# Kernel tuning notes

Measured on AMD Instinct MI355X. Metric: run time of the kernel, lower is better.

Reference implementation:

```python
import jax, jax.numpy as jnp
import numpy as np

B, T = 64, 256
IN, HID, OUT = 512, 1024, 256
NUM_DOMAINS = 20

def setup_inputs() -> dict:
    key = jax.random.key(0)
    k1, k2, k3, k4 = jax.random.split(key, 4)
    x = jax.random.normal(k1, (B, T, IN), dtype=jnp.float32)
    hetero_info = jax.random.randint(k2, (B, 2), 0, NUM_DOMAINS, dtype=jnp.int64)
    # embedding tables init N(0, 0.02) as in the torch module
    fc1_table = 0.02 * jax.random.normal(k3, (NUM_DOMAINS, IN * HID + HID), dtype=jnp.float32)
    fc2_table = 0.02 * jax.random.normal(k4, (NUM_DOMAINS, HID * OUT + OUT), dtype=jnp.float32)
    return {"x": x, "hetero_info": hetero_info, "fc1_table": fc1_table, "fc2_table": fc2_table}

def reference(x, hetero_info, fc1_table, fc2_table):
    domain_id = hetero_info[:, 0].astype(jnp.int32)
    Bn = domain_id.shape[0]
    fc1_param = fc1_table[domain_id]                     # (B, IN*HID + HID)
    w1 = fc1_param[:, : IN * HID].reshape(Bn, IN, HID)   # (B, IN, HID)
    b1 = fc1_param[:, IN * HID:].reshape(Bn, 1, HID)
    fc2_param = fc2_table[domain_id]                     # (B, HID*OUT + OUT)
    w2 = fc2_param[:, : HID * OUT].reshape(Bn, HID, OUT) # (B, HID, OUT)
    b2 = fc2_param[:, HID * OUT:].reshape(Bn, 1, OUT)
    h = jnp.einsum('bti,bih->bth', x, w1) + b1
    h = jax.nn.gelu(h, approximate=False)  # torch nn.GELU default = exact erf
    out = jnp.einsum('bth,bho->bto', h, w2) + b2
    return out
```

## Files before the change

kernel.cpp:

```cpp
#include <hip/hip_runtime.h>
#include <math.h>

#define B_  64
#define T_  256
#define IN_ 512
#define HID_ 1024
#define OUT_ 256
#define NDOM 20

typedef __bf16 bf16_t;
typedef __bf16 bf16x8 __attribute__((ext_vector_type(8)));
typedef float  f32x4  __attribute__((ext_vector_type(4)));

#define LSTR 40

__device__ __forceinline__ unsigned f2bf_bits(float f) {
    unsigned u = __builtin_bit_cast(unsigned, f);
    return (u + 0x7FFFu + ((u >> 16) & 1u)) >> 16;
}
__device__ __forceinline__ unsigned pack_bf16x2(float x, float y) {
    return f2bf_bits(x) | (f2bf_bits(y) << 16);
}

template<int K, int N>
__global__ __launch_bounds__(256) void cvt_transpose(
    const float* __restrict__ table,
    bf16_t*      __restrict__ Wt,
    float*       __restrict__ BiasOut)
{
    const int d  = blockIdx.z;
    const float* W = table + (size_t)d * ((size_t)K * N + N);
    const int n0 = blockIdx.x * 64;
    const int k0 = blockIdx.y * 64;
    const int tid = threadIdx.x;

    __shared__ float t[64][65];

    #pragma unroll
    for (int r = 0; r < 4; ++r) {
        const int kl = (tid >> 4) + r * 16;
        const int nl = (tid & 15) * 4;
        float4 v = *(const float4*)(W + (size_t)(k0 + kl) * N + n0 + nl);
        t[kl][nl + 0] = v.x; t[kl][nl + 1] = v.y;
        t[kl][nl + 2] = v.z; t[kl][nl + 3] = v.w;
    }
    __syncthreads();

    bf16_t* Wtd = Wt + (size_t)d * K * N;
    #pragma unroll
    for (int r = 0; r < 4; ++r) {
        const int nl = (tid >> 4) + r * 16;
        const int k4 = (tid & 15) * 4;
        uint2 p;
        p.x = pack_bf16x2(t[k4 + 0][nl], t[k4 + 1][nl]);
        p.y = pack_bf16x2(t[k4 + 2][nl], t[k4 + 3][nl]);
        *(uint2*)(Wtd + (size_t)(n0 + nl) * K + k0 + k4) = p;
    }

    if (blockIdx.y == 0 && tid < 64)
        BiasOut[(size_t)d * N + n0 + tid] = W[(size_t)K * N + n0 + tid];
}

template<int N_ALL, int K, int BM, int BN, bool GELU, bool A_BF16, typename OUT_T>
__global__ __launch_bounds__(256) void mfma_bgemm(
    const void*   __restrict__ Ain,
    const bf16_t* __restrict__ Wt,
    const float*  __restrict__ Bias,
    const int*    __restrict__ hetero,
    OUT_T*        __restrict__ Out)
{
    constexpr int FI = BM / 32;
    constexpr int FJ = BN / 32;

    const int b = blockIdx.z;
    const int d = hetero[2 * b];
    const bf16_t* W    = Wt + (size_t)d * N_ALL * K;
    const float*  bias = Bias + (size_t)d * N_ALL;

    const int n0 = blockIdx.x * BN;
    const int m0 = blockIdx.y * BM;

    __shared__ bf16_t LdsA[BM * LSTR];
    __shared__ bf16_t LdsB[BN * LSTR];

    const int tid  = threadIdx.x;
    const int wave = tid >> 6;
    const int lane = tid & 63;
    const int l16  = lane & 15;
    const int quad = lane >> 4;
    const int wm   = (wave >> 1) * (BM / 2);
    const int wn   = (wave & 1) * (BN / 2);

    f32x4 acc[FI][FJ] = {};

    for (int kk = 0; kk < K; kk += 32) {
        if constexpr (A_BF16) {
            const bf16_t* A = (const bf16_t*)Ain + (size_t)b * 256 * K;
            const int kc = (tid & 3) * 8;
            #pragma unroll
            for (int r = 0; r < BM / 64; ++r) {
                const int m = (tid >> 2) + r * 64;
                *(uint4*)&LdsA[m * LSTR + kc] =
                    *(const uint4*)(A + (size_t)(m0 + m) * K + kk + kc);
            }
        } else {
            const float* A = (const float*)Ain + (size_t)b * 256 * K;
            const int kc = (tid & 7) * 4;
            #pragma unroll
            for (int r = 0; r < BM / 32; ++r) {
                const int m = (tid >> 3) + r * 32;
                float4 v = *(const float4*)(A + (size_t)(m0 + m) * K + kk + kc);
                uint2 p;
                p.x = pack_bf16x2(v.x, v.y);
                p.y = pack_bf16x2(v.z, v.w);
                *(uint2*)&LdsA[m * LSTR + kc] = p;
            }
        }
        {
            const int kc = (tid & 3) * 8;
            #pragma unroll
            for (int r = 0; r < BN / 64; ++r) {
                const int n = (tid >> 2) + r * 64;
                *(uint4*)&LdsB[n * LSTR + kc] =
                    *(const uint4*)(W + (size_t)(n0 + n) * K + kk + kc);
            }
        }
        __syncthreads();

        bf16x8 af[FI], bfg[FJ];
        #pragma unroll
        for (int i = 0; i < FI; ++i)
            af[i] = *(const bf16x8*)&LdsA[(wm + i * 16 + l16) * LSTR + quad * 8];
        #pragma unroll
        for (int j = 0; j < FJ; ++j)
            bfg[j] = *(const bf16x8*)&LdsB[(wn + j * 16 + l16) * LSTR + quad * 8];
        #pragma unroll
        for (int i = 0; i < FI; ++i)
            #pragma unroll
            for (int j = 0; j < FJ; ++j)
                acc[i][j] = __builtin_amdgcn_mfma_f32_16x16x32_bf16(af[i], bfg[j], acc[i][j], 0, 0, 0);
        __syncthreads();
    }

    #pragma unroll
    for (int j = 0; j < FJ; ++j) {
        const int n = n0 + wn + j * 16 + l16;
        const float bia = bias[n];
        #pragma unroll
        for (int i = 0; i < FI; ++i) {
            const int mbase = m0 + wm + i * 16 + quad * 4;
            #pragma unroll
            for (int r = 0; r < 4; ++r) {
                float vv = acc[i][j][r] + bia;
                if (GELU) vv = 0.5f * vv * (1.0f + erff(vv * 0.70710678f));
                Out[(size_t)b * 256 * N_ALL + (size_t)(mbase + r) * N_ALL + n] = (OUT_T)vv;
            }
        }
    }
}

extern "C" void kernel_launch(void* const* d_in, const int* in_sizes, int n_in,
                              void* d_out, int out_size, void* d_ws, size_t ws_size,
                              hipStream_t stream) {
    const float* x         = (const float*)d_in[0];
    const int*   hetero    = (const int*)d_in[1];
    const float* fc1_table = (const float*)d_in[2];
    const float* fc2_table = (const float*)d_in[3];
    float*       out       = (float*)d_out;

    char* ws = (char*)d_ws;
    bf16_t* W1t = (bf16_t*)(ws);
    bf16_t* W2t = (bf16_t*)(ws + 20971520);
    float*  b1  = (float*)(ws + 31457280);
    float*  b2  = (float*)(ws + 31539200);
    bf16_t* H   = (bf16_t*)(ws + 31559680);

    cvt_transpose<IN_, HID_><<<dim3(HID_ / 64, IN_ / 64, NDOM), 256, 0, stream>>>(
        fc1_table, W1t, b1);
    cvt_transpose<HID_, OUT_><<<dim3(OUT_ / 64, HID_ / 64, NDOM), 256, 0, stream>>>(
        fc2_table, W2t, b2);

    mfma_bgemm<HID_, IN_, 128, 128, true, false, bf16_t>
        <<<dim3(HID_ / 128, T_ / 128, B_), 256, 0, stream>>>(x, W1t, b1, hetero, H);

    mfma_bgemm<OUT_, HID_, 64, 64, false, true, float>
        <<<dim3(OUT_ / 64, T_ / 64, B_), 256, 0, stream>>>(H, W2t, b2, hetero, out);
}
```

Measured before the change: 213.2 us.

## Use direct global-to-LDS loads with XOR-swizzled layouts and remapped grids

Both GEMMs now stage their tiles with global_load_lds (direct global-to-LDS DMA), so the data no longer passes through registers. The LDS layouts use XOR swizzles in place of padded strides, which is meant to avoid bank conflicts. fc1 keeps x in fp32 in LDS and converts to bf16 when building the MFMA fragments. fc2 now uses a K-step of 64, and both kernels use a 1D grid ordered so consecutive blocks share the same n-tile (weight tile) across batches. The trade-off is that fc1 uses more LDS for the fp32 A tile and repeats the bf16 conversion in each wave.

```diff
diff --git a/kernel.cpp b/kernel.cpp
--- a/kernel.cpp
+++ b/kernel.cpp
@@ -12,8 +12,6 @@
 typedef __bf16 bf16x8 __attribute__((ext_vector_type(8)));
 typedef float  f32x4  __attribute__((ext_vector_type(4)));
 
-#define LSTR 40
-
 __device__ __forceinline__ unsigned f2bf_bits(float f) {
     unsigned u = __builtin_bit_cast(unsigned, f);
     return (u + 0x7FFFu + ((u >> 16) & 1u)) >> 16;
@@ -22,11 +20,16 @@
     return f2bf_bits(x) | (f2bf_bits(y) << 16);
 }
 
+__device__ __forceinline__ void gl_lds16(const void* g, void* l) {
+    __builtin_amdgcn_global_load_lds(
+        (const __attribute__((address_space(1))) unsigned*)g,
+        (__attribute__((address_space(3))) unsigned*)l,
+        16, 0, 0);
+}
+
 template<int K, int N>
 __global__ __launch_bounds__(256) void cvt_transpose(
-    const float* __restrict__ table,
-    bf16_t*      __restrict__ Wt,
-    float*       __restrict__ BiasOut)
+    const float* __restrict__ table, bf16_t* __restrict__ Wt, float* __restrict__ BiasOut)
 {
     const int d  = blockIdx.z;
     const float* W = table + (size_t)d * ((size_t)K * N + N);
@@ -61,99 +64,184 @@
         BiasOut[(size_t)d * N + n0 + tid] = W[(size_t)K * N + n0 + tid];
 }
 
-template<int N_ALL, int K, int BM, int BN, bool GELU, bool A_BF16, typename OUT_T>
-__global__ __launch_bounds__(256) void mfma_bgemm(
-    const void*   __restrict__ Ain,
-    const bf16_t* __restrict__ Wt,
+__global__ __launch_bounds__(256) void fc1_gemm(
+    const float*  __restrict__ X,
+    const bf16_t* __restrict__ W1t,
     const float*  __restrict__ Bias,
     const int*    __restrict__ hetero,
-    OUT_T*        __restrict__ Out)
+    bf16_t*       __restrict__ H)
 {
-    constexpr int FI = BM / 32;
-    constexpr int FJ = BN / 32;
-
-    const int b = blockIdx.z;
-    const int d = hetero[2 * b];
-    const bf16_t* W    = Wt + (size_t)d * N_ALL * K;
-    const float*  bias = Bias + (size_t)d * N_ALL;
-
-    const int n0 = blockIdx.x * BN;
-    const int m0 = blockIdx.y * BM;
-
-    __shared__ bf16_t LdsA[BM * LSTR];
-    __shared__ bf16_t LdsB[BN * LSTR];
+    const int id   = blockIdx.x;
+    const int g    = id & 127;
+    const int nidx = id >> 7;
+    const int b    = g >> 1;
+    const int m0   = (g & 1) * 128;
+    const int n0   = nidx * 128;
+    const int d    = hetero[2 * b];
+    const bf16_t* W    = W1t + (size_t)d * HID_ * IN_;
+    const float*  bias = Bias + (size_t)d * HID_;
+
+    __shared__ __attribute__((aligned(16))) float  LdsA[128 * 32];
+    __shared__ __attribute__((aligned(16))) bf16_t LdsB[128 * 32];
 
     const int tid  = threadIdx.x;
     const int wave = tid >> 6;
     const int lane = tid & 63;
     const int l16  = lane & 15;
     const int quad = lane >> 4;
-    const int wm   = (wave >> 1) * (BM / 2);
-    const int wn   = (wave & 1) * (BN / 2);
-
-    f32x4 acc[FI][FJ] = {};
-
-    for (int kk = 0; kk < K; kk += 32) {
-        if constexpr (A_BF16) {
-            const bf16_t* A = (const bf16_t*)Ain + (size_t)b * 256 * K;
-            const int kc = (tid & 3) * 8;
-            #pragma unroll
-            for (int r = 0; r < BM / 64; ++r) {
-                const int m = (tid >> 2) + r * 64;
-                *(uint4*)&LdsA[m * LSTR + kc] =
-                    *(const uint4*)(A + (size_t)(m0 + m) * K + kk + kc);
-            }
-        } else {
-            const float* A = (const float*)Ain + (size_t)b * 256 * K;
-            const int kc = (tid & 7) * 4;
-            #pragma unroll
-            for (int r = 0; r < BM / 32; ++r) {
-                const int m = (tid >> 3) + r * 32;
-                float4 v = *(const float4*)(A + (size_t)(m0 + m) * K + kk + kc);
-                uint2 p;
-                p.x = pack_bf16x2(v.x, v.y);
-                p.y = pack_bf16x2(v.z, v.w);
-                *(uint2*)&LdsA[m * LSTR + kc] = p;
-            }
-        }
-        {
-            const int kc = (tid & 3) * 8;
-            #pragma unroll
-            for (int r = 0; r < BN / 64; ++r) {
-                const int n = (tid >> 2) + r * 64;
-                *(uint4*)&LdsB[n * LSTR + kc] =
-                    *(const uint4*)(W + (size_t)(n0 + n) * K + kk + kc);
-            }
-        }
-        __syncthreads();
-
-        bf16x8 af[FI], bfg[FJ];
-        #pragma unroll
-        for (int i = 0; i < FI; ++i)
-            af[i] = *(const bf16x8*)&LdsA[(wm + i * 16 + l16) * LSTR + quad * 8];
-        #pragma unroll
-        for (int j = 0; j < FJ; ++j)
-            bfg[j] = *(const bf16x8*)&LdsB[(wn + j * 16 + l16) * LSTR + quad * 8];
-        #pragma unroll
-        for (int i = 0; i < FI; ++i)
-            #pragma unroll
-            for (int j = 0; j < FJ; ++j)
+    const int wm   = (wave >> 1) * 64;
+    const int wn   = (wave & 1) * 64;
+
+    f32x4 acc[4][4] = {};
+
+    for (int kk = 0; kk < IN_; kk += 32) {
+        #pragma unroll
+        for (int cc = 0; cc < 4; ++cc) {
+            const int r0  = wave * 32 + cc * 8;
+            const int row = r0 + (lane >> 3);
+            const int cs  = (lane & 7) ^ (row & 7);
+            gl_lds16(X + ((size_t)(b * 256 + m0 + row) * IN_ + kk + cs * 4),
+                     &LdsA[r0 * 32]);
+        }
+        #pragma unroll
+        for (int cc = 0; cc < 2; ++cc) {
+            const int r0  = wave * 32 + cc * 16;
+            const int row = r0 + (lane >> 2);
+            const int cs  = (lane & 3) ^ ((row >> 1) & 3);
+            gl_lds16(W + (size_t)(n0 + row) * IN_ + kk + cs * 8,
+                     &LdsB[r0 * 32]);
+        }
+        __syncthreads();
+
+        bf16x8 af[4], bfg[4];
+        #pragma unroll
+        for (int i = 0; i < 4; ++i) {
+            const int r  = wm + i * 16 + l16;
+            const int c0 = (quad * 2)     ^ (r & 7);
+            const int c1 = (quad * 2 + 1) ^ (r & 7);
+            float4 f0 = *(const float4*)&LdsA[r * 32 + c0 * 4];
+            float4 f1 = *(const float4*)&LdsA[r * 32 + c1 * 4];
+            union { bf16x8 v; unsigned u[4]; } a;
+            a.u[0] = pack_bf16x2(f0.x, f0.y);
+            a.u[1] = pack_bf16x2(f0.z, f0.w);
+            a.u[2] = pack_bf16x2(f1.x, f1.y);
+            a.u[3] = pack_bf16x2(f1.z, f1.w);
+            af[i] = a.v;
+        }
+        #pragma unroll
+        for (int j = 0; j < 4; ++j) {
+            const int r  = wn + j * 16 + l16;
+            const int cB = quad ^ ((r >> 1) & 3);
+            bfg[j] = *(const bf16x8*)&LdsB[r * 32 + cB * 8];
+        }
+        #pragma unroll
+        for (int i = 0; i < 4; ++i)
+            #pragma unroll
+            for (int j = 0; j < 4; ++j)
                 acc[i][j] = __builtin_amdgcn_mfma_f32_16x16x32_bf16(af[i], bfg[j], acc[i][j], 0, 0, 0);
         __syncthreads();
     }
 
     #pragma unroll
-    for (int j = 0; j < FJ; ++j) {
+    for (int j = 0; j < 4; ++j) {
         const int n = n0 + wn + j * 16 + l16;
         const float bia = bias[n];
         #pragma unroll
-        for (int i = 0; i < FI; ++i) {
+        for (int i = 0; i < 4; ++i) {
             const int mbase = m0 + wm + i * 16 + quad * 4;
             #pragma unroll
             for (int r = 0; r < 4; ++r) {
                 float vv = acc[i][j][r] + bia;
-                if (GELU) vv = 0.5f * vv * (1.0f + erff(vv * 0.70710678f));
-                Out[(size_t)b * 256 * N_ALL + (size_t)(mbase + r) * N_ALL + n] = (OUT_T)vv;
+                vv = 0.5f * vv * (1.0f + erff(vv * 0.70710678f));
+                H[((size_t)b * 256 + mbase + r) * HID_ + n] = (bf16_t)vv;
+            }
+        }
+    }
+}
+
+__global__ __launch_bounds__(256) void fc2_gemm(
+    const bf16_t* __restrict__ H,
+    const bf16_t* __restrict__ W2t,
+    const float*  __restrict__ Bias,
+    const int*    __restrict__ hetero,
+    float*        __restrict__ Out)
+{
+    const int id   = blockIdx.x;
+    const int g    = id & 255;
+    const int nidx = id >> 8;
+    const int b    = g >> 2;
+    const int m0   = (g & 3) * 64;
+    const int n0   = nidx * 64;
+    const int d    = hetero[2 * b];
+    const bf16_t* W    = W2t + (size_t)d * OUT_ * HID_;
+    const float*  bias = Bias + (size_t)d * OUT_;
+
+    __shared__ __attribute__((aligned(16))) bf16_t LdsA[64 * 64];
+    __shared__ __attribute__((aligned(16))) bf16_t LdsB[64 * 64];
+
+    const int tid  = threadIdx.x;
+    const int wave = tid >> 6;
+    const int lane = tid & 63;
+    const int l16  = lane & 15;
+    const int quad = lane >> 4;
+    const int wm   = (wave >> 1) * 32;
+    const int wn   = (wave & 1) * 32;
+
+    f32x4 acc[2][2] = {};
+
+    for (int kk = 0; kk < HID_; kk += 64) {
+        #pragma unroll
+        for (int cc = 0; cc < 2; ++cc) {
+            const int r0  = wave * 16 + cc * 8;
+            const int row = r0 + (lane >> 3);
+            const int cs  = (lane & 7) ^ (row & 7);
+            gl_lds16(H + (size_t)(b * 256 + m0 + row) * HID_ + kk + cs * 8,
+                     &LdsA[r0 * 64]);
+        }
+        #pragma unroll
+        for (int cc = 0; cc < 2; ++cc) {
+            const int r0  = wave * 16 + cc * 8;
+            const int row = r0 + (lane >> 3);
+            const int cs  = (lane & 7) ^ (row & 7);
+            gl_lds16(W + (size_t)(n0 + row) * HID_ + kk + cs * 8,
+                     &LdsB[r0 * 64]);
+        }
+        __syncthreads();
+
+        #pragma unroll
+        for (int h = 0; h < 2; ++h) {
+            bf16x8 af[2], bfg[2];
+            #pragma unroll
+            for (int i = 0; i < 2; ++i) {
+                const int r = wm + i * 16 + l16;
+                const int c = (h * 4 + quad) ^ (r & 7);
+                af[i] = *(const bf16x8*)&LdsA[r * 64 + c * 8];
+            }
+            #pragma unroll
+            for (int j = 0; j < 2; ++j) {
+                const int r = wn + j * 16 + l16;
+                const int c = (h * 4 + quad) ^ (r & 7);
+                bfg[j] = *(const bf16x8*)&LdsB[r * 64 + c * 8];
+            }
+            #pragma unroll
+            for (int i = 0; i < 2; ++i)
+                #pragma unroll
+                for (int j = 0; j < 2; ++j)
+                    acc[i][j] = __builtin_amdgcn_mfma_f32_16x16x32_bf16(af[i], bfg[j], acc[i][j], 0, 0, 0);
+        }
+        __syncthreads();
+    }
+
+    #pragma unroll
+    for (int j = 0; j < 2; ++j) {
+        const int n = n0 + wn + j * 16 + l16;
+        const float bia = bias[n];
+        #pragma unroll
+        for (int i = 0; i < 2; ++i) {
+            const int mbase = m0 + wm + i * 16 + quad * 4;
+            #pragma unroll
+            for (int r = 0; r < 4; ++r) {
+                Out[((size_t)b * 256 + mbase + r) * OUT_ + n] = acc[i][j][r] + bia;
             }
         }
     }
@@ -180,9 +268,6 @@
     cvt_transpose<HID_, OUT_><<<dim3(OUT_ / 64, HID_ / 64, NDOM), 256, 0, stream>>>(
         fc2_table, W2t, b2);
 
-    mfma_bgemm<HID_, IN_, 128, 128, true, false, bf16_t>
-        <<<dim3(HID_ / 128, T_ / 128, B_), 256, 0, stream>>>(x, W1t, b1, hetero, H);
-
-    mfma_bgemm<OUT_, HID_, 64, 64, false, true, float>
-        <<<dim3(OUT_ / 64, T_ / 64, B_), 256, 0, stream>>>(H, W2t, b2, hetero, out);
-}
+    fc1_gemm<<<dim3(1024), 256, 0, stream>>>(x, W1t, b1, hetero, H);
+    fc2_gemm<<<dim3(1024), 256, 0, stream>>>(H, W2t, b2, hetero, out);
+}
```

Result: faster. 193.1 us (-9.4%).
